# Kernel tuning notes

Measured on AMD Instinct MI355X. Metric: run time of the kernel, lower is better.

## Reference

```python
import jax, jax.numpy as jnp
import numpy as np

NUM_TRACKS = [5313, 1643, 128, 0]
MAX_TRACKS = max(NUM_TRACKS)
EMBED_DIM = 1536
LN_EPS = 1e-5


def setup_inputs() -> dict:
    key = jax.random.key(0)
    ks = jax.random.split(key, 8)
    B, S, D = 4, 896, EMBED_DIM
    inp = {
        "x": jax.random.normal(ks[0], (B, S, D), dtype=jnp.float32),
        "head_idx": jax.random.randint(ks[1], (B,), 0, 4, dtype=jnp.int64) if jax.config.jax_enable_x64 else jax.random.randint(ks[1], (B,), 0, 4).astype(jnp.int32),
    }
    for i, n in enumerate([5313, 1643, 128]):
        inp[f"gamma{i}"] = jnp.ones((D,), jnp.float32)
        inp[f"beta{i}"] = jnp.zeros((D,), jnp.float32)
        inp[f"W{i}"] = jax.random.normal(ks[2 + i], (n, D), dtype=jnp.float32) * 0.02
        inp[f"b{i}"] = jnp.zeros((n,), jnp.float32)
    return inp


def _linear_head(x, gamma, beta, W, b):
    # LayerNormFP32 -> Linear -> softplus, cast back to orig dtype
    orig_dtype = x.dtype
    xf = x.astype(jnp.float32)
    mu = jnp.mean(xf, axis=-1, keepdims=True)
    var = jnp.var(xf, axis=-1, keepdims=True)  # biased, as torch LayerNorm
    xn = (xf - mu) * jax.lax.rsqrt(var + LN_EPS) * gamma + beta
    h = jax.nn.softplus(jnp.einsum("bsd,td->bst", xn, W) + b)
    return h.astype(orig_dtype)


def reference(x, head_idx, gamma0, beta0, W0, b0,
              gamma1, beta1, W1, b1, gamma2, beta2, W2, b2):
    params = [(gamma0, beta0, W0, b0),
              (gamma1, beta1, W1, b1),
              (gamma2, beta2, W2, b2),
              None]  # ZeroHead
    B, S, _ = x.shape
    logits = jnp.zeros((B, S, MAX_TRACKS), dtype=x.dtype)
    for i, p in enumerate(params):
        if p is None:
            padded = jnp.zeros((B, S, MAX_TRACKS), dtype=x.dtype)
        else:
            h = _linear_head(x, *p)  # [B, S, n_i]
            pad = MAX_TRACKS - h.shape[-1]
            padded = jnp.pad(h, ((0, 0), (0, 0), (0, pad))) if pad > 0 else h
        mask = (head_idx == i)[:, None, None]
        logits = jnp.where(mask, padded, logits)
    return logits
```

## Files before the change

### kernel.cpp

```cpp
#include <hip/hip_runtime.h>
#include <hip/hip_bf16.h>

#define EMBED 1536
#define SEQ   896
#define NOUT  5313

#define N0 5313
#define N1 1643
#define N2 128
#define W0OFF 0
#define W1OFF 5376
#define W2OFF 7040
#define PTOT  7168

#define LN_BLOCKS 1792
#define WC_BLOCKS 5376
#define GEMM_GRID 1280
#define BK 64
#define NKT (EMBED / BK)

typedef __attribute__((ext_vector_type(8))) short bf16x8;
typedef __attribute__((ext_vector_type(4))) float f32x4;

__device__ __forceinline__ void gload_lds16(const void* g, void* l) {
    __builtin_amdgcn_global_load_lds(
        (const __attribute__((address_space(1))) void*)g,
        (__attribute__((address_space(3))) void*)l, 16, 0, 0);
}

__device__ __forceinline__ int tiles_of(int h) {
    return (h == 0) ? 42 : (h == 1) ? 13 : (h == 2) ? 1 : 0;
}
__device__ __forceinline__ int nrows_of(int h) {
    return (h == 0) ? N0 : (h == 1) ? N1 : (h == 2) ? N2 : 0;
}

__global__ __launch_bounds__(256) void prep_kernel(
    const float* __restrict__ x, const int* __restrict__ head_idx,
    const float* __restrict__ g0, const float* __restrict__ be0,
    const float* __restrict__ g1, const float* __restrict__ be1,
    const float* __restrict__ g2, const float* __restrict__ be2,
    const float* __restrict__ W0, const float* __restrict__ W1,
    const float* __restrict__ W2,
    __hip_bfloat16* __restrict__ xn, __hip_bfloat16* __restrict__ wpad)
{
    const int tid = threadIdx.x;

    if (blockIdx.x < LN_BLOCKS) {
        const int half = tid >> 7;
        const int lt   = tid & 127;
        const int row  = blockIdx.x * 2 + half;
        const int b    = row / SEQ;
        const int h    = head_idx[b];
        if (h == 3) return;

        const float* gamma = (h == 1) ? g1 : (h == 2) ? g2 : g0;
        const float* beta  = (h == 1) ? be1 : (h == 2) ? be2 : be0;
        const float* xr = x + (size_t)row * EMBED;

        float4 v[3];
        float sum = 0.f, sq = 0.f;
#pragma unroll
        for (int i = 0; i < 3; ++i) {
            v[i] = ((const float4*)xr)[lt + i * 128];
            sum += v[i].x + v[i].y + v[i].z + v[i].w;
            sq  += v[i].x * v[i].x + v[i].y * v[i].y + v[i].z * v[i].z + v[i].w * v[i].w;
        }
#pragma unroll
        for (int off = 32; off > 0; off >>= 1) {
            sum += __shfl_down(sum, off);
            sq  += __shfl_down(sq, off);
        }
        __shared__ float s_sum[4], s_sq[4];
        const int wave = tid >> 6, lane = tid & 63;
        if (lane == 0) { s_sum[wave] = sum; s_sq[wave] = sq; }
        __syncthreads();
        const int wb = half << 1;
        const float mu  = (s_sum[wb] + s_sum[wb + 1]) * (1.f / EMBED);
        const float var = (s_sq[wb] + s_sq[wb + 1]) * (1.f / EMBED) - mu * mu;
        const float rs  = rsqrtf(var + 1e-5f);

        __hip_bfloat16* xo = xn + (size_t)row * EMBED;
#pragma unroll
        for (int i = 0; i < 3; ++i) {
            const int idx = lt + i * 128;
            float4 gv = ((const float4*)gamma)[idx];
            float4 bv = ((const float4*)beta)[idx];
            union { __hip_bfloat16 h4[4]; short4 s4; } u;
            u.h4[0] = __float2bfloat16((v[i].x - mu) * rs * gv.x + bv.x);
            u.h4[1] = __float2bfloat16((v[i].y - mu) * rs * gv.y + bv.y);
            u.h4[2] = __float2bfloat16((v[i].z - mu) * rs * gv.z + bv.z);
            u.h4[3] = __float2bfloat16((v[i].w - mu) * rs * gv.w + bv.w);
            ((short4*)xo)[idx] = u.s4;
        }
    } else {
        const int gid = (blockIdx.x - LN_BLOCKS) * 256 + tid;
        const int r = gid / 192;
        const int c = (gid - r * 192) * 8;
        const int region = (r < W1OFF) ? 0 : (r < W2OFF) ? 1 : 2;
        const int h0 = head_idx[0], h1 = head_idx[1];
        const int h2 = head_idx[2], h3 = head_idx[3];
        if (region != h0 && region != h1 && region != h2 && region != h3)
            return;
        const float* src = nullptr;
        if (region == 0)      { if (r < N0) src = W0 + (size_t)r * EMBED; }
        else if (region == 1) { int rr = r - W1OFF; if (rr < N1) src = W1 + (size_t)rr * EMBED; }
        else                  { int rr = r - W2OFF; if (rr < N2) src = W2 + (size_t)rr * EMBED; }
        union { __hip_bfloat16 h8[8]; int4 v4; } u;
        if (src) {
            float4 a = ((const float4*)(src + c))[0];
            float4 b = ((const float4*)(src + c))[1];
            u.h8[0] = __float2bfloat16(a.x); u.h8[1] = __float2bfloat16(a.y);
            u.h8[2] = __float2bfloat16(a.z); u.h8[3] = __float2bfloat16(a.w);
            u.h8[4] = __float2bfloat16(b.x); u.h8[5] = __float2bfloat16(b.y);
            u.h8[6] = __float2bfloat16(b.z); u.h8[7] = __float2bfloat16(b.w);
        } else {
            u.v4 = make_int4(0, 0, 0, 0);
        }
        *(int4*)(wpad + (size_t)r * EMBED + c) = u.v4;
    }
}

__global__ __launch_bounds__(256, 2) void head_gemm(
    const __hip_bfloat16* __restrict__ xn,
    const __hip_bfloat16* __restrict__ wpad,
    const float* __restrict__ b0, const float* __restrict__ b1,
    const float* __restrict__ b2,
    const int* __restrict__ head_idx,
    float* __restrict__ out)
{
    const int h0 = head_idx[0], h1 = head_idx[1];
    const int h2 = head_idx[2], h3 = head_idx[3];
    const int t0 = tiles_of(h0) * 7, t1 = tiles_of(h1) * 7;
    const int t2 = tiles_of(h2) * 7, t3 = tiles_of(h3) * 7;
    const int R = t0 + t1 + t2 + t3;
    const int tid = threadIdx.x;

    if ((int)blockIdx.x >= R) {
        const int j = blockIdx.x - R;
        const int ZB = GEMM_GRID - R;
        for (int row = j; row < 4 * SEQ; row += ZB) {
            const int b = row / SEQ;
            const int h = (b == 0) ? h0 : (b == 1) ? h1 : (b == 2) ? h2 : h3;
            const int n = nrows_of(h);
            if (n >= NOUT) continue;
            float* o = out + (size_t)row * NOUT;
            const int pre0 = (4 - (int)(((size_t)row * NOUT + n) & 3)) & 3;
            const int pre_end = min(n + pre0, NOUT);
            for (int c = n + tid; c < pre_end; c += 256) o[c] = 0.f;
            const int nvec = (NOUT - pre_end) >> 2;
            const float4 z = make_float4(0.f, 0.f, 0.f, 0.f);
            float4* ov = (float4*)(o + pre_end);
            for (int i = tid; i < nvec; i += 256) ov[i] = z;
            for (int c = pre_end + (nvec << 2) + tid; c < NOUT; c += 256) o[c] = 0.f;
        }
        return;
    }

    const int q = R >> 3, r7 = R & 7;
    const int xcd = (int)blockIdx.x & 7, jx = (int)blockIdx.x >> 3;
    const int tile = (xcd < r7 ? xcd * (q + 1) : r7 * (q + 1) + (xcd - r7) * q) + jx;

    int rem = tile, b;
    if (rem < t0)                { b = 0; }
    else if (rem < t0 + t1)      { b = 1; rem -= t0; }
    else if (rem < t0 + t1 + t2) { b = 2; rem -= t0 + t1; }
    else                         { b = 3; rem -= t0 + t1 + t2; }

    const int h = (b == 0) ? h0 : (b == 1) ? h1 : (b == 2) ? h2 : h3;
    const int nt = rem / 7;
    const int mt = rem - nt * 7;
    const int nrows = nrows_of(h);
    const int wbase = (h == 0) ? W0OFF : (h == 1) ? W1OFF : W2OFF;

    const int col0 = nt * 128;
    float* outb = out + ((size_t)b * SEQ + (size_t)mt * 128) * NOUT;

    __shared__ __hip_bfloat16 As[2][128 * BK];
    __shared__ __hip_bfloat16 Bs[2][128 * BK];
    const __hip_bfloat16* Ab = xn + ((size_t)b * SEQ + (size_t)mt * 128) * EMBED;
    const __hip_bfloat16* Bb = wpad + (size_t)(wbase + col0) * EMBED;

    const int wave = tid >> 6, lane = tid & 63;
    const int wm = wave >> 1, wn = wave & 1;
    const int fm = lane & 15, quad = lane >> 4;

    auto stage = [&](int buf, int kt) {
        const int k0 = kt * BK;
#pragma unroll
        for (int i = 0; i < 4; ++i) {
            const int c = tid + i * 256;
            const int arow = c >> 3;
            const int kc = (c & 7) ^ (arow & 7);
            gload_lds16(Ab + (size_t)arow * EMBED + k0 + kc * 8, &As[buf][c * 8]);
        }
#pragma unroll
        for (int i = 0; i < 4; ++i) {
            const int c = tid + i * 256;
            const int brow = c >> 3;
            const int kc = (c & 7) ^ (brow & 7);
            gload_lds16(Bb + (size_t)brow * EMBED + k0 + kc * 8, &Bs[buf][c * 8]);
        }
    };

    f32x4 acc[4][4] = {};

    stage(0, 0);
    stage(1, 1);

    for (int kt = 0; kt < NKT; ++kt) {
        const int cur = kt & 1;
        if (kt + 1 < NKT)
            asm volatile("s_waitcnt vmcnt(8)" ::: "memory");
        else
            asm volatile("s_waitcnt vmcnt(0)" ::: "memory");
        __builtin_amdgcn_s_barrier();
#pragma unroll
        for (int ks = 0; ks < 2; ++ks) {
            bf16x8 af[4], bfr[4];
#pragma unroll
            for (int i = 0; i < 4; ++i)
                af[i] = *(const bf16x8*)&As[cur][(wm * 64 + i * 16 + fm) * BK +
                                                ((((ks << 2) + quad)) ^ (fm & 7)) * 8];
#pragma unroll
            for (int j2 = 0; j2 < 4; ++j2)
                bfr[j2] = *(const bf16x8*)&Bs[cur][(wn * 64 + j2 * 16 + fm) * BK +
                                                  ((((ks << 2) + quad)) ^ (fm & 7)) * 8];
#pragma unroll
            for (int i = 0; i < 4; ++i)
#pragma unroll
                for (int j2 = 0; j2 < 4; ++j2)
                    acc[i][j2] = __builtin_amdgcn_mfma_f32_16x16x32_bf16(
                        af[i], bfr[j2], acc[i][j2], 0, 0, 0);
        }
        __builtin_amdgcn_s_barrier();
        if (kt + 2 < NKT) stage(cur, kt + 2);
    }

    const float* bias = (h == 1) ? b1 : (h == 2) ? b2 : b0;
#pragma unroll
    for (int j = 0; j < 4; ++j) {
        const int lcol = col0 + wn * 64 + j * 16 + fm;
        const bool valid = lcol < nrows;
        const float bv = valid ? bias[lcol] : 0.f;
#pragma unroll
        for (int i = 0; i < 4; ++i) {
            const int rbase = wm * 64 + i * 16 + quad * 4;
#pragma unroll
            for (int r = 0; r < 4; ++r) {
                const float v = acc[i][j][r] + bv;
                const float sp = fmaxf(v, 0.f) + __logf(1.f + __expf(-fabsf(v)));
                if (valid) outb[(size_t)(rbase + r) * NOUT + lcol] = sp;
            }
        }
    }
}

extern "C" void kernel_launch(void* const* d_in, const int* in_sizes, int n_in,
                              void* d_out, int out_size, void* d_ws, size_t ws_size,
                              hipStream_t stream) {
    const float* x   = (const float*)d_in[0];
    const int* hidx  = (const int*)d_in[1];
    const float* g0  = (const float*)d_in[2];
    const float* be0 = (const float*)d_in[3];
    const float* W0  = (const float*)d_in[4];
    const float* b0  = (const float*)d_in[5];
    const float* g1  = (const float*)d_in[6];
    const float* be1 = (const float*)d_in[7];
    const float* W1  = (const float*)d_in[8];
    const float* b1  = (const float*)d_in[9];
    const float* g2  = (const float*)d_in[10];
    const float* be2 = (const float*)d_in[11];
    const float* W2  = (const float*)d_in[12];
    const float* b2  = (const float*)d_in[13];
    float* out = (float*)d_out;

    const size_t XN_BYTES = (size_t)4 * SEQ * EMBED * 2;
    __hip_bfloat16* xn   = (__hip_bfloat16*)d_ws;
    __hip_bfloat16* wpad = (__hip_bfloat16*)((char*)d_ws + XN_BYTES);

    prep_kernel<<<LN_BLOCKS + WC_BLOCKS, 256, 0, stream>>>(
        x, hidx, g0, be0, g1, be1, g2, be2, W0, W1, W2, xn, wpad);
    head_gemm<<<GEMM_GRID, 256, 0, stream>>>(xn, wpad, b0, b1, b2, hidx, out);
}
```

Measured before the change: 171.6 us.

## Fuse fp32 weight-to-bf16 conversion into GEMM B-tile staging

Removes the separate weight conversion pass that wrote a padded bf16 copy of the weights. The GEMM now loads fp32 weights into registers, converts them to bf16 and writes them to LDS, with register prefetch of the next tile. This drops the extra write and read of the bf16 weight buffer. In exchange every M-tile rereads fp32 weights (twice the bytes, seven times over), and B staging no longer uses direct-to-LDS loads, adding register pressure and a full __syncthreads per k-step.

```diff
diff --git a/kernel.cpp b/kernel.cpp
--- a/kernel.cpp
+++ b/kernel.cpp
@@ -8,13 +8,8 @@
 #define N0 5313
 #define N1 1643
 #define N2 128
-#define W0OFF 0
-#define W1OFF 5376
-#define W2OFF 7040
-#define PTOT  7168
 
 #define LN_BLOCKS 1792
-#define WC_BLOCKS 5376
 #define GEMM_GRID 1280
 #define BK 64
 #define NKT (EMBED / BK)
@@ -40,90 +35,61 @@
     const float* __restrict__ g0, const float* __restrict__ be0,
     const float* __restrict__ g1, const float* __restrict__ be1,
     const float* __restrict__ g2, const float* __restrict__ be2,
-    const float* __restrict__ W0, const float* __restrict__ W1,
-    const float* __restrict__ W2,
-    __hip_bfloat16* __restrict__ xn, __hip_bfloat16* __restrict__ wpad)
+    __hip_bfloat16* __restrict__ xn)
 {
     const int tid = threadIdx.x;
-
-    if (blockIdx.x < LN_BLOCKS) {
-        const int half = tid >> 7;
-        const int lt   = tid & 127;
-        const int row  = blockIdx.x * 2 + half;
-        const int b    = row / SEQ;
-        const int h    = head_idx[b];
-        if (h == 3) return;
-
-        const float* gamma = (h == 1) ? g1 : (h == 2) ? g2 : g0;
-        const float* beta  = (h == 1) ? be1 : (h == 2) ? be2 : be0;
-        const float* xr = x + (size_t)row * EMBED;
-
-        float4 v[3];
-        float sum = 0.f, sq = 0.f;
-#pragma unroll
-        for (int i = 0; i < 3; ++i) {
-            v[i] = ((const float4*)xr)[lt + i * 128];
-            sum += v[i].x + v[i].y + v[i].z + v[i].w;
-            sq  += v[i].x * v[i].x + v[i].y * v[i].y + v[i].z * v[i].z + v[i].w * v[i].w;
-        }
-#pragma unroll
-        for (int off = 32; off > 0; off >>= 1) {
-            sum += __shfl_down(sum, off);
-            sq  += __shfl_down(sq, off);
-        }
-        __shared__ float s_sum[4], s_sq[4];
-        const int wave = tid >> 6, lane = tid & 63;
-        if (lane == 0) { s_sum[wave] = sum; s_sq[wave] = sq; }
-        __syncthreads();
-        const int wb = half << 1;
-        const float mu  = (s_sum[wb] + s_sum[wb + 1]) * (1.f / EMBED);
-        const float var = (s_sq[wb] + s_sq[wb + 1]) * (1.f / EMBED) - mu * mu;
-        const float rs  = rsqrtf(var + 1e-5f);
-
-        __hip_bfloat16* xo = xn + (size_t)row * EMBED;
-#pragma unroll
-        for (int i = 0; i < 3; ++i) {
-            const int idx = lt + i * 128;
-            float4 gv = ((const float4*)gamma)[idx];
-            float4 bv = ((const float4*)beta)[idx];
-            union { __hip_bfloat16 h4[4]; short4 s4; } u;
-            u.h4[0] = __float2bfloat16((v[i].x - mu) * rs * gv.x + bv.x);
-            u.h4[1] = __float2bfloat16((v[i].y - mu) * rs * gv.y + bv.y);
-            u.h4[2] = __float2bfloat16((v[i].z - mu) * rs * gv.z + bv.z);
-            u.h4[3] = __float2bfloat16((v[i].w - mu) * rs * gv.w + bv.w);
-            ((short4*)xo)[idx] = u.s4;
-        }
-    } else {
-        const int gid = (blockIdx.x - LN_BLOCKS) * 256 + tid;
-        const int r = gid / 192;
-        const int c = (gid - r * 192) * 8;
-        const int region = (r < W1OFF) ? 0 : (r < W2OFF) ? 1 : 2;
-        const int h0 = head_idx[0], h1 = head_idx[1];
-        const int h2 = head_idx[2], h3 = head_idx[3];
-        if (region != h0 && region != h1 && region != h2 && region != h3)
-            return;
-        const float* src = nullptr;
-        if (region == 0)      { if (r < N0) src = W0 + (size_t)r * EMBED; }
-        else if (region == 1) { int rr = r - W1OFF; if (rr < N1) src = W1 + (size_t)rr * EMBED; }
-        else                  { int rr = r - W2OFF; if (rr < N2) src = W2 + (size_t)rr * EMBED; }
-        union { __hip_bfloat16 h8[8]; int4 v4; } u;
-        if (src) {
-            float4 a = ((const float4*)(src + c))[0];
-            float4 b = ((const float4*)(src + c))[1];
-            u.h8[0] = __float2bfloat16(a.x); u.h8[1] = __float2bfloat16(a.y);
-            u.h8[2] = __float2bfloat16(a.z); u.h8[3] = __float2bfloat16(a.w);
-            u.h8[4] = __float2bfloat16(b.x); u.h8[5] = __float2bfloat16(b.y);
-            u.h8[6] = __float2bfloat16(b.z); u.h8[7] = __float2bfloat16(b.w);
-        } else {
-            u.v4 = make_int4(0, 0, 0, 0);
-        }
-        *(int4*)(wpad + (size_t)r * EMBED + c) = u.v4;
+    const int half = tid >> 7;
+    const int lt   = tid & 127;
+    const int row  = blockIdx.x * 2 + half;
+    const int b    = row / SEQ;
+    const int h    = head_idx[b];
+    if (h == 3) return;
+
+    const float* gamma = (h == 1) ? g1 : (h == 2) ? g2 : g0;
+    const float* beta  = (h == 1) ? be1 : (h == 2) ? be2 : be0;
+    const float* xr = x + (size_t)row * EMBED;
+
+    float4 v[3];
+    float sum = 0.f, sq = 0.f;
+#pragma unroll
+    for (int i = 0; i < 3; ++i) {
+        v[i] = ((const float4*)xr)[lt + i * 128];
+        sum += v[i].x + v[i].y + v[i].z + v[i].w;
+        sq  += v[i].x * v[i].x + v[i].y * v[i].y + v[i].z * v[i].z + v[i].w * v[i].w;
+    }
+#pragma unroll
+    for (int off = 32; off > 0; off >>= 1) {
+        sum += __shfl_down(sum, off);
+        sq  += __shfl_down(sq, off);
+    }
+    __shared__ float s_sum[4], s_sq[4];
+    const int wave = tid >> 6, lane = tid & 63;
+    if (lane == 0) { s_sum[wave] = sum; s_sq[wave] = sq; }
+    __syncthreads();
+    const int wb = half << 1;
+    const float mu  = (s_sum[wb] + s_sum[wb + 1]) * (1.f / EMBED);
+    const float var = (s_sq[wb] + s_sq[wb + 1]) * (1.f / EMBED) - mu * mu;
+    const float rs  = rsqrtf(var + 1e-5f);
+
+    __hip_bfloat16* xo = xn + (size_t)row * EMBED;
+#pragma unroll
+    for (int i = 0; i < 3; ++i) {
+        const int idx = lt + i * 128;
+        float4 gv = ((const float4*)gamma)[idx];
+        float4 bv = ((const float4*)beta)[idx];
+        union { __hip_bfloat16 h4[4]; short4 s4; } u;
+        u.h4[0] = __float2bfloat16((v[i].x - mu) * rs * gv.x + bv.x);
+        u.h4[1] = __float2bfloat16((v[i].y - mu) * rs * gv.y + bv.y);
+        u.h4[2] = __float2bfloat16((v[i].z - mu) * rs * gv.z + bv.z);
+        u.h4[3] = __float2bfloat16((v[i].w - mu) * rs * gv.w + bv.w);
+        ((short4*)xo)[idx] = u.s4;
     }
 }
 
 __global__ __launch_bounds__(256, 2) void head_gemm(
     const __hip_bfloat16* __restrict__ xn,
-    const __hip_bfloat16* __restrict__ wpad,
+    const float* __restrict__ W0f, const float* __restrict__ W1f,
+    const float* __restrict__ W2f,
     const float* __restrict__ b0, const float* __restrict__ b1,
     const float* __restrict__ b2,
     const int* __restrict__ head_idx,
@@ -171,7 +137,7 @@
     const int nt = rem / 7;
     const int mt = rem - nt * 7;
     const int nrows = nrows_of(h);
-    const int wbase = (h == 0) ? W0OFF : (h == 1) ? W1OFF : W2OFF;
+    const float* Wf = (h == 1) ? W1f : (h == 2) ? W2f : W0f;
 
     const int col0 = nt * 128;
     float* outb = out + ((size_t)b * SEQ + (size_t)mt * 128) * NOUT;
@@ -179,13 +145,12 @@
     __shared__ __hip_bfloat16 As[2][128 * BK];
     __shared__ __hip_bfloat16 Bs[2][128 * BK];
     const __hip_bfloat16* Ab = xn + ((size_t)b * SEQ + (size_t)mt * 128) * EMBED;
-    const __hip_bfloat16* Bb = wpad + (size_t)(wbase + col0) * EMBED;
 
     const int wave = tid >> 6, lane = tid & 63;
     const int wm = wave >> 1, wn = wave & 1;
     const int fm = lane & 15, quad = lane >> 4;
 
-    auto stage = [&](int buf, int kt) {
+    auto stageA = [&](int buf, int kt) {
         const int k0 = kt * BK;
 #pragma unroll
         for (int i = 0; i < 4; ++i) {
@@ -194,27 +159,58 @@
             const int kc = (c & 7) ^ (arow & 7);
             gload_lds16(Ab + (size_t)arow * EMBED + k0 + kc * 8, &As[buf][c * 8]);
         }
-#pragma unroll
-        for (int i = 0; i < 4; ++i) {
-            const int c = tid + i * 256;
+    };
+
+    float4 bld[4][2];
+    auto stageB_load = [&](int kt) {
+        const int k0 = kt * BK;
+#pragma unroll
+        for (int r = 0; r < 4; ++r) {
+            const int c = tid + r * 256;
             const int brow = c >> 3;
             const int kc = (c & 7) ^ (brow & 7);
-            gload_lds16(Bb + (size_t)brow * EMBED + k0 + kc * 8, &Bs[buf][c * 8]);
+            const int w = col0 + brow;
+            if (w < nrows) {
+                const float4* src = (const float4*)(Wf + (size_t)w * EMBED + k0 + kc * 8);
+                bld[r][0] = src[0];
+                bld[r][1] = src[1];
+            } else {
+                bld[r][0] = make_float4(0.f, 0.f, 0.f, 0.f);
+                bld[r][1] = make_float4(0.f, 0.f, 0.f, 0.f);
+            }
         }
     };
+    auto stageB_write = [&](int buf) {
+#pragma unroll
+        for (int r = 0; r < 4; ++r) {
+            const int c = tid + r * 256;
+            union { __hip_bfloat16 h8[8]; int4 v4; } u;
+            u.h8[0] = __float2bfloat16(bld[r][0].x);
+            u.h8[1] = __float2bfloat16(bld[r][0].y);
+            u.h8[2] = __float2bfloat16(bld[r][0].z);
+            u.h8[3] = __float2bfloat16(bld[r][0].w);
+            u.h8[4] = __float2bfloat16(bld[r][1].x);
+            u.h8[5] = __float2bfloat16(bld[r][1].y);
+            u.h8[6] = __float2bfloat16(bld[r][1].z);
+            u.h8[7] = __float2bfloat16(bld[r][1].w);
+            *(int4*)&Bs[buf][c * 8] = u.v4;
+        }
+    };
 
     f32x4 acc[4][4] = {};
 
-    stage(0, 0);
-    stage(1, 1);
+    stageB_load(0);
+    stageA(0, 0);
+    stageB_write(0);
+    __syncthreads();
 
     for (int kt = 0; kt < NKT; ++kt) {
         const int cur = kt & 1;
-        if (kt + 1 < NKT)
-            asm volatile("s_waitcnt vmcnt(8)" ::: "memory");
-        else
-            asm volatile("s_waitcnt vmcnt(0)" ::: "memory");
-        __builtin_amdgcn_s_barrier();
+        const bool more = (kt + 1 < NKT);
+        if (more) {
+            stageB_load(kt + 1);
+            stageA(cur ^ 1, kt + 1);
+        }
 #pragma unroll
         for (int ks = 0; ks < 2; ++ks) {
             bf16x8 af[4], bfr[4];
@@ -233,8 +229,8 @@
                     acc[i][j2] = __builtin_amdgcn_mfma_f32_16x16x32_bf16(
                         af[i], bfr[j2], acc[i][j2], 0, 0, 0);
         }
-        __builtin_amdgcn_s_barrier();
-        if (kt + 2 < NKT) stage(cur, kt + 2);
+        if (more) stageB_write(cur ^ 1);
+        __syncthreads();
     }
 
     const float* bias = (h == 1) ? b1 : (h == 2) ? b2 : b0;
@@ -275,11 +271,10 @@
     const float* b2  = (const float*)d_in[13];
     float* out = (float*)d_out;
 
-    const size_t XN_BYTES = (size_t)4 * SEQ * EMBED * 2;
-    __hip_bfloat16* xn   = (__hip_bfloat16*)d_ws;
-    __hip_bfloat16* wpad = (__hip_bfloat16*)((char*)d_ws + XN_BYTES);
-
-    prep_kernel<<<LN_BLOCKS + WC_BLOCKS, 256, 0, stream>>>(
-        x, hidx, g0, be0, g1, be1, g2, be2, W0, W1, W2, xn, wpad);
-    head_gemm<<<GEMM_GRID, 256, 0, stream>>>(xn, wpad, b0, b1, b2, hidx, out);
-}
+    __hip_bfloat16* xn = (__hip_bfloat16*)d_ws;
+
+    prep_kernel<<<LN_BLOCKS, 256, 0, stream>>>(
+        x, hidx, g0, be0, g1, be1, g2, be2, xn);
+    head_gemm<<<GEMM_GRID, 256, 0, stream>>>(
+        xn, W0, W1, W2, b0, b1, b2, hidx, out);
+}
```

New measurement: 221.8 us. 1.29x slower.
